# Kernel tuning notes

Hardware: AMD Instinct MI355X
Metric: run time of the kernel (lower is better)

The kernel has to match this reference:

```python
import jax, jax.numpy as jnp
import numpy as np

N = 100_000   # nodes
E = 1_600_000 # edges (avg degree 16)
D = 128       # numeric_dim
H = 128       # hidden_dim
C = 2         # num_classes
EPS = 1e-5    # BatchNorm eps


def setup_inputs() -> dict:
    key = jax.random.key(0)
    ks = jax.random.split(key, 24)

    def lin(k, i, o):  # torch Linear init-ish, stored as [in, out]
        return (jax.random.normal(k, (i, o), jnp.float32) / np.sqrt(i)).astype(jnp.float32)

    inp = {
        "x": jax.random.normal(ks[0], (N, D), jnp.float32),
        "edge_index": jax.random.randint(ks[1], (2, E), 0, N),
        "in_w": lin(ks[2], D, H),
        "in_b": jnp.zeros((H,), jnp.float32),
        "cls_w": lin(ks[3], H, C),
        "cls_b": jnp.zeros((C,), jnp.float32),
    }
    k = 4
    for blk in ("b1", "b2", "b3"):
        inp[f"{blk}_lw"] = lin(ks[k + 0], H, H)      # SAGEConv lin_l (aggregated neighbors), has bias
        inp[f"{blk}_lb"] = jnp.zeros((H,), jnp.float32)
        inp[f"{blk}_rw"] = lin(ks[k + 1], H, H)      # SAGEConv lin_r (root), bias=False in PyG
        inp[f"{blk}_g"] = jnp.ones((H,), jnp.float32)   # BN gamma
        inp[f"{blk}_bt"] = jnp.zeros((H,), jnp.float32)  # BN beta
        k += 2
    return inp


def _sage_block(x, src, dst, lw, lb, rw, g, bt):
    # SAGEConv with mean aggregation: messages flow src -> dst
    agg = jax.ops.segment_sum(x[src], dst, num_segments=N)            # [N, H]
    deg = jax.ops.segment_sum(jnp.ones((src.shape[0], 1), x.dtype), dst, num_segments=N)
    mean = agg / jnp.maximum(deg, 1.0)
    out = mean @ lw + lb + x @ rw                                     # lin_l(mean) + lin_r(x)
    # BatchNorm1d (training-mode batch stats over nodes), biased variance
    mu = out.mean(axis=0)
    var = out.var(axis=0)
    out = (out - mu) * jax.lax.rsqrt(var + EPS) * g + bt
    out = jax.nn.relu(out)
    # dropout in eval mode = identity; skip is Identity (H == H)
    return out + x


def reference(x, edge_index, in_w, in_b, cls_w, cls_b,
              b1_lw, b1_lb, b1_rw, b1_g, b1_bt,
              b2_lw, b2_lb, b2_rw, b2_g, b2_bt,
              b3_lw, b3_lb, b3_rw, b3_g, b3_bt):
    src, dst = edge_index[0], edge_index[1]
    h = jax.nn.relu(x @ in_w + in_b)
    h = _sage_block(h, src, dst, b1_lw, b1_lb, b1_rw, b1_g, b1_bt)
    h = _sage_block(h, src, dst, b2_lw, b2_lb, b2_rw, b2_g, b2_bt)
    h = _sage_block(h, src, dst, b3_lw, b3_lb, b3_rw, b3_g, b3_bt)
    return h @ cls_w + cls_b  # [N, C] logits
```

## Files before the change

### kernel.cpp

```cpp
#include <hip/hip_runtime.h>

#define NN 100000
#define NE 1600000
#define HD 128
#define EPSI 1e-5f

using u32 = unsigned int;
using u16 = unsigned short;

typedef short bf16x8 __attribute__((ext_vector_type(8)));
typedef float f32x4  __attribute__((ext_vector_type(4)));
typedef u32   u32x4  __attribute__((ext_vector_type(4)));

constexpr int SCAN_CHUNK  = 1024;
constexpr int SCAN_BLOCKS = (NN + SCAN_CHUNK - 1) / SCAN_CHUNK;
constexpr int NRANGE      = 128;
constexpr int RSZ2        = 784;
constexpr int BINCAP      = 16384;
constexpr int PART_CHUNK4 = 1024;
constexpr int PART_GRID   = (NE / 4 + PART_CHUNK4 - 1) / PART_CHUNK4;

__device__ inline float bflo(u32 u) { return __uint_as_float(u << 16); }
__device__ inline float bfhi(u32 u) { return __uint_as_float(u & 0xFFFF0000u); }
__device__ inline u16 f2bf(float f) {
    u32 u = __float_as_uint(f);
    u += 0x7FFFu + ((u >> 16) & 1u);
    return (u16)(u >> 16);
}
__device__ inline u32 pack2(float a, float b) {
    return (u32)f2bf(a) | ((u32)f2bf(b) << 16);
}


__global__ __launch_bounds__(256) void k_part(const int* __restrict__ src,
                                              const int* __restrict__ dst,
                                              int* __restrict__ binCur,
                                              u32* __restrict__ binbuf) {
    __shared__ int hist[NRANGE], base[NRANGE], curs[NRANGE];
    const int t  = threadIdx.x;
    const int c0 = blockIdx.x * PART_CHUNK4;
    if (t < NRANGE) { hist[t] = 0; curs[t] = 0; }
    __syncthreads();

    int4 ds[4], ss[4];
    bool ok[4];
#pragma unroll
    for (int i = 0; i < 4; ++i) {
        const int c = c0 + t + 256 * i;
        ok[i] = c < NE / 4;
        if (ok[i]) {
            ds[i] = reinterpret_cast<const int4*>(dst)[c];
            ss[i] = reinterpret_cast<const int4*>(src)[c];
        }
    }
#pragma unroll
    for (int i = 0; i < 4; ++i) {
        if (ok[i]) {
            atomicAdd(&hist[ds[i].x / RSZ2], 1);
            atomicAdd(&hist[ds[i].y / RSZ2], 1);
            atomicAdd(&hist[ds[i].z / RSZ2], 1);
            atomicAdd(&hist[ds[i].w / RSZ2], 1);
        }
    }
    __syncthreads();
    if (t < NRANGE && hist[t] > 0) base[t] = atomicAdd(&binCur[t], hist[t]);
    __syncthreads();

#pragma unroll
    for (int i = 0; i < 4; ++i) {
        if (ok[i]) {
            const int d[4] = {ds[i].x, ds[i].y, ds[i].z, ds[i].w};
            const int s[4] = {ss[i].x, ss[i].y, ss[i].z, ss[i].w};
#pragma unroll
            for (int j = 0; j < 4; ++j) {
                const int r  = d[j] / RSZ2;
                const int ld = d[j] - r * RSZ2;
                const int p  = base[r] + atomicAdd(&curs[r], 1);
                if (p < BINCAP)
                    binbuf[(size_t)r * BINCAP + p] = ((u32)s[j] << 10) | (u32)ld;
            }
        }
    }
}

__global__ __launch_bounds__(1024) void k_countL(const int* __restrict__ binCur,
                                                 const u32* __restrict__ binbuf,
                                                 int* __restrict__ cnt) {
    __shared__ int hist[RSZ2];
    const int b = blockIdx.x;
    const int t = threadIdx.x;
    for (int i = t; i < RSZ2; i += 1024) hist[i] = 0;
    __syncthreads();
    const int n = min(binCur[b], BINCAP);
    const u32* bin = binbuf + (size_t)b * BINCAP;
    for (int i = t; i < n; i += 1024)
        atomicAdd(&hist[bin[i] & 1023u], 1);
    __syncthreads();
    for (int i = t; i < RSZ2; i += 1024) {
        const int idx = b * RSZ2 + i;
        if (idx < NN) cnt[idx] = hist[i];
    }
}

__global__ void k_scan1(const int* __restrict__ cnt, int* __restrict__ rp,
                        int* __restrict__ tot) {
    __shared__ int lds[256];
    const int t    = threadIdx.x;
    const int base = blockIdx.x * SCAN_CHUNK + t * 4;
    int v[4];
#pragma unroll
    for (int i = 0; i < 4; ++i) v[i] = (base + i < NN) ? cnt[base + i] : 0;
    const int s = v[0] + v[1] + v[2] + v[3];
    lds[t] = s;
    __syncthreads();
    int val = s;
    for (int off = 1; off < 256; off <<= 1) {
        int other = (t >= off) ? lds[t - off] : 0;
        __syncthreads();
        val += other;
        lds[t] = val;
        __syncthreads();
    }
    int e = val - s;
#pragma unroll
    for (int i = 0; i < 4; ++i) {
        if (base + i < NN) rp[base + i] = e;
        e += v[i];
    }
    if (t == 255) tot[blockIdx.x] = val;
}

__global__ void k_scan2(int* __restrict__ tot, int* __restrict__ rp) {
    __shared__ int l[128];
    const int t = threadIdx.x;
    const int v = (t < SCAN_BLOCKS) ? tot[t] : 0;
    l[t] = v;
    __syncthreads();
    int val = v;
    for (int off = 1; off < 128; off <<= 1) {
        const int o = (t >= off) ? l[t - off] : 0;
        __syncthreads();
        val += o;
        l[t] = val;
        __syncthreads();
    }
    if (t < SCAN_BLOCKS) tot[t] = val - v;
    if (t == 127) rp[NN] = val;
}

__global__ void k_scan3(int* __restrict__ rp, const int* __restrict__ tot) {
    int idx = blockIdx.x * 256 + threadIdx.x;
    if (idx < NN) rp[idx] += tot[idx >> 10];
}

__global__ __launch_bounds__(1024) void k_fillL(const int* __restrict__ binCur,
                                                const u32* __restrict__ binbuf,
                                                const int* __restrict__ rp,
                                                int* __restrict__ col) {
    __shared__ int cur[RSZ2];
    const int b = blockIdx.x;
    const int t = threadIdx.x;
    for (int i = t; i < RSZ2; i += 1024) {
        const int idx = b * RSZ2 + i;
        cur[i] = (idx < NN) ? rp[idx] : 0;
    }
    __syncthreads();
    const int n = min(binCur[b], BINCAP);
    const u32* bin = binbuf + (size_t)b * BINCAP;
    for (int i = t; i < n; i += 1024) {
        const u32 e = bin[i];
        col[atomicAdd(&cur[e & 1023u], 1)] = (int)(e >> 10);
    }
}


struct WTArgs { const float* w[7]; u16* o[7]; };

__global__ void k_wt(WTArgs a) {
    const int m = blockIdx.y;
    const int n = blockIdx.x;
    const int k = threadIdx.x;
    a.o[m][n * HD + k] = f2bf(a.w[m][k * HD + n]);
}


__device__ inline void acc8(float* a, u32x4 v) {
    a[0] += bflo(v.x); a[1] += bfhi(v.x);
    a[2] += bflo(v.y); a[3] += bfhi(v.y);
    a[4] += bflo(v.z); a[5] += bfhi(v.z);
    a[6] += bflo(v.w); a[7] += bfhi(v.w);
}

__global__ __launch_bounds__(256) void k_agg(const u16* __restrict__ h,
                                             const int* __restrict__ rp,
                                             const int* __restrict__ col,
                                             u16* __restrict__ mean) {
    const int lane = threadIdx.x & 63;
    const int node = blockIdx.x * 4 + (threadIdx.x >> 6);
    const int grp  = lane >> 4;
    const int li   = lane & 15;
    const int r0 = rp[node], r1 = rp[node + 1];
    const size_t lof = (size_t)li * 8;
    float a[8];
#pragma unroll
    for (int i = 0; i < 8; ++i) a[i] = 0.f;
    int e = r0 + grp;
    for (; e + 12 < r1; e += 16) {
        const int s0 = col[e], s1 = col[e + 4], s2 = col[e + 8], s3 = col[e + 12];
        const u32x4 v0 = *reinterpret_cast<const u32x4*>(&h[(size_t)s0 * HD + lof]);
        const u32x4 v1 = *reinterpret_cast<const u32x4*>(&h[(size_t)s1 * HD + lof]);
        const u32x4 v2 = *reinterpret_cast<const u32x4*>(&h[(size_t)s2 * HD + lof]);
        const u32x4 v3 = *reinterpret_cast<const u32x4*>(&h[(size_t)s3 * HD + lof]);
        acc8(a, v0); acc8(a, v1); acc8(a, v2); acc8(a, v3);
    }
    for (; e < r1; e += 4) {
        const u32x4 v = *reinterpret_cast<const u32x4*>(&h[(size_t)col[e] * HD + lof]);
        acc8(a, v);
    }
#pragma unroll
    for (int i = 0; i < 8; ++i) {
        a[i] += __shfl_xor(a[i], 16);
        a[i] += __shfl_xor(a[i], 32);
    }
    if (lane < 16) {
        const float inv = 1.0f / fmaxf((float)(r1 - r0), 1.0f);
        u32x4 o;
        o.x = pack2(a[0] * inv, a[1] * inv);
        o.y = pack2(a[2] * inv, a[3] * inv);
        o.z = pack2(a[4] * inv, a[5] * inv);
        o.w = pack2(a[6] * inv, a[7] * inv);
        *reinterpret_cast<u32x4*>(&mean[(size_t)node * HD + lof]) = o;
    }
}


template <int A1F32, int RELU, int STATS>
__global__ __launch_bounds__(256) void k_mgemm(
    const void* __restrict__ A1p, const u16* __restrict__ W1T,
    const u16* __restrict__ A2, const u16* __restrict__ W2T,
    const float* __restrict__ bias, u16* __restrict__ out,
    float* __restrict__ stats)
{
    __shared__ u32x4 Wlds[2048];
    const int t    = threadIdx.x;
    const int wv   = t >> 6;
    const int lane = t & 63;
    const int lid  = lane & 15;
    const int kseg = lane >> 4;
    const int row0 = blockIdx.x * 128 + wv * 32;

    f32x4 acc[2][8];
#pragma unroll
    for (int rf = 0; rf < 2; ++rf)
#pragma unroll
        for (int c = 0; c < 8; ++c) acc[rf][c] = (f32x4){0.f, 0.f, 0.f, 0.f};

    int  ar[2];
    bool rok[2];
#pragma unroll
    for (int rf = 0; rf < 2; ++rf) {
        ar[rf]  = row0 + rf * 16 + lid;
        rok[rf] = ar[rf] < NN;
    }

#pragma unroll
    for (int i = 0; i < 8; ++i) {
        const int g   = t + 256 * i;
        const int row = g >> 4;
        const int ch  = g & 15;
        Wlds[row * 16 + (ch ^ (row & 7))] = reinterpret_cast<const u32x4*>(W1T)[g];
    }
    u32x4 wreg[8];
    if (A2 != nullptr) {
#pragma unroll
        for (int i = 0; i < 8; ++i)
            wreg[i] = reinterpret_cast<const u32x4*>(W2T)[t + 256 * i];
    }

    bf16x8 af1[2][4], af2[2][4];
    if (A1F32) {
        const float* A = (const float*)A1p;
#pragma unroll
        for (int rf = 0; rf < 2; ++rf)
#pragma unroll
            for (int kk = 0; kk < 4; ++kk) {
                const int kof = kk * 32 + kseg * 8;
                if (rok[rf]) {
                    const float4 f0 = *reinterpret_cast<const float4*>(&A[(size_t)ar[rf] * HD + kof]);
                    const float4 f1 = *reinterpret_cast<const float4*>(&A[(size_t)ar[rf] * HD + kof + 4]);
                    af1[rf][kk][0] = (short)f2bf(f0.x); af1[rf][kk][1] = (short)f2bf(f0.y);
                    af1[rf][kk][2] = (short)f2bf(f0.z); af1[rf][kk][3] = (short)f2bf(f0.w);
                    af1[rf][kk][4] = (short)f2bf(f1.x); af1[rf][kk][5] = (short)f2bf(f1.y);
                    af1[rf][kk][6] = (short)f2bf(f1.z); af1[rf][kk][7] = (short)f2bf(f1.w);
                } else {
                    af1[rf][kk] = (bf16x8)0;
                }
            }
    } else {
        const u16* A = (const u16*)A1p;
#pragma unroll
        for (int rf = 0; rf < 2; ++rf)
#pragma unroll
            for (int kk = 0; kk < 4; ++kk) {
                const int kof = kk * 32 + kseg * 8;
                af1[rf][kk] = rok[rf]
                    ? *reinterpret_cast<const bf16x8*>(&A[(size_t)ar[rf] * HD + kof])
                    : (bf16x8)0;
            }
    }
    if (A2 != nullptr) {
#pragma unroll
        for (int rf = 0; rf < 2; ++rf)
#pragma unroll
            for (int kk = 0; kk < 4; ++kk) {
                const int kof = kk * 32 + kseg * 8;
                af2[rf][kk] = rok[rf]
                    ? *reinterpret_cast<const bf16x8*>(&A2[(size_t)ar[rf] * HD + kof])
                    : (bf16x8)0;
            }
    }

    __syncthreads();
#pragma unroll
    for (int kk = 0; kk < 4; ++kk) {
#pragma unroll
        for (int c = 0; c < 8; ++c) {
            const int brow = c * 16 + lid;
            const bf16x8 bf = *reinterpret_cast<const bf16x8*>(
                &Wlds[brow * 16 + ((kk * 4 + kseg) ^ (lid & 7))]);
#pragma unroll
            for (int rf = 0; rf < 2; ++rf)
                acc[rf][c] = __builtin_amdgcn_mfma_f32_16x16x32_bf16(af1[rf][kk], bf, acc[rf][c], 0, 0, 0);
        }
    }

    if (A2 != nullptr) {
        __syncthreads();
#pragma unroll
        for (int i = 0; i < 8; ++i) {
            const int g   = t + 256 * i;
            const int row = g >> 4;
            const int ch  = g & 15;
            Wlds[row * 16 + (ch ^ (row & 7))] = wreg[i];
        }
        __syncthreads();
#pragma unroll
        for (int kk = 0; kk < 4; ++kk) {
#pragma unroll
            for (int c = 0; c < 8; ++c) {
                const int brow = c * 16 + lid;
                const bf16x8 bf = *reinterpret_cast<const bf16x8*>(
                    &Wlds[brow * 16 + ((kk * 4 + kseg) ^ (lid & 7))]);
#pragma unroll
                for (int rf = 0; rf < 2; ++rf)
                    acc[rf][c] = __builtin_amdgcn_mfma_f32_16x16x32_bf16(af2[rf][kk], bf, acc[rf][c], 0, 0, 0);
            }
        }
    }

    float bv[8];
#pragma unroll
    for (int c = 0; c < 8; ++c) bv[c] = bias[c * 16 + lid];

    float sv[8], qv[8];
#pragma unroll
    for (int c = 0; c < 8; ++c) { sv[c] = 0.f; qv[c] = 0.f; }

#pragma unroll
    for (int rf = 0; rf < 2; ++rf) {
#pragma unroll
        for (int c = 0; c < 8; ++c) {
            const int colc = c * 16 + lid;
#pragma unroll
            for (int j = 0; j < 4; ++j) {
                const int rrow = row0 + rf * 16 + kseg * 4 + j;
                if (rrow < NN) {
                    float o = acc[rf][c][j] + bv[c];
                    if (RELU) o = fmaxf(o, 0.f);
                    out[(size_t)rrow * HD + colc] = f2bf(o);
                    sv[c] += o;
                    qv[c] += o * o;
                }
            }
        }
    }

    if constexpr (STATS) {
        __shared__ float ls[4][HD], lq[4][HD];
#pragma unroll
        for (int c = 0; c < 8; ++c) {
            sv[c] += __shfl_xor(sv[c], 16);
            sv[c] += __shfl_xor(sv[c], 32);
            qv[c] += __shfl_xor(qv[c], 16);
            qv[c] += __shfl_xor(qv[c], 32);
        }
        if (lane < 16) {
#pragma unroll
            for (int c = 0; c < 8; ++c) {
                ls[wv][c * 16 + lid] = sv[c];
                lq[wv][c * 16 + lid] = qv[c];
            }
        }
        __syncthreads();
        if (t < HD) {
            const float s = (ls[0][t] + ls[1][t]) + (ls[2][t] + ls[3][t]);
            atomicAdd(&stats[t], s);
        } else {
            const int j = t - HD;
            const float q = (lq[0][j] + lq[1][j]) + (lq[2][j] + lq[3][j]);
            atomicAdd(&stats[HD + j], q);
        }
    }
}


template <int CLS>
__global__ __launch_bounds__(256) void k_apply(
    const u16* __restrict__ outb, const float* __restrict__ stats,
    const float* __restrict__ g, const float* __restrict__ bt,
    u16* __restrict__ hb, const float* __restrict__ cw,
    const float* __restrict__ cb, float* __restrict__ logits)
{
    const int t = threadIdx.x;
    const size_t idx4 = (size_t)blockIdx.x * 256 + t;
    const int j = (int)(idx4 & 31) * 4;
    const float4 svv = *reinterpret_cast<const float4*>(&stats[j]);
    const float4 qvv = *reinterpret_cast<const float4*>(&stats[HD + j]);
    const float4 gv  = *reinterpret_cast<const float4*>(&g[j]);
    const float4 bv  = *reinterpret_cast<const float4*>(&bt[j]);
    const float invn = 1.0f / (float)NN;
    float sc[4], sh[4];
    {
        const float sa[4] = {svv.x, svv.y, svv.z, svv.w};
        const float qa[4] = {qvv.x, qvv.y, qvv.z, qvv.w};
        const float ga[4] = {gv.x, gv.y, gv.z, gv.w};
        const float ba[4] = {bv.x, bv.y, bv.z, bv.w};
#pragma unroll
        for (int i = 0; i < 4; ++i) {
            const float mean = sa[i] * invn;
            const float var  = qa[i] * invn - mean * mean;
            sc[i] = ga[i] * rsqrtf(var + EPSI);
            sh[i] = ba[i] - mean * sc[i];
        }
    }
    const uint2 o  = reinterpret_cast<const uint2*>(outb)[idx4];
    const uint2 hv = reinterpret_cast<const uint2*>(hb)[idx4];
    const float r0 = fmaxf(bflo(o.x) * sc[0] + sh[0], 0.f) + bflo(hv.x);
    const float r1 = fmaxf(bfhi(o.x) * sc[1] + sh[1], 0.f) + bfhi(hv.x);
    const float r2 = fmaxf(bflo(o.y) * sc[2] + sh[2], 0.f) + bflo(hv.y);
    const float r3 = fmaxf(bfhi(o.y) * sc[3] + sh[3], 0.f) + bfhi(hv.y);
    reinterpret_cast<uint2*>(hb)[idx4] = make_uint2(pack2(r0, r1), pack2(r2, r3));

    if constexpr (CLS) {
        const float4 w01 = *reinterpret_cast<const float4*>(&cw[j * 2]);
        const float4 w23 = *reinterpret_cast<const float4*>(&cw[j * 2 + 4]);
        float p0 = r0 * w01.x + r1 * w01.z + r2 * w23.x + r3 * w23.z;
        float p1 = r0 * w01.y + r1 * w01.w + r2 * w23.y + r3 * w23.w;
#pragma unroll
        for (int off = 1; off <= 16; off <<= 1) {
            p0 += __shfl_xor(p0, off);
            p1 += __shfl_xor(p1, off);
        }
        if ((t & 31) == 0) {
            const size_t row = idx4 >> 5;
            logits[row * 2 + 0] = p0 + cb[0];
            logits[row * 2 + 1] = p1 + cb[1];
        }
    }
}


extern "C" void kernel_launch(void* const* d_in, const int* in_sizes, int n_in,
                              void* d_out, int out_size, void* d_ws, size_t ws_size,
                              hipStream_t stream) {
    const float* x     = (const float*)d_in[0];
    const int*   ei    = (const int*)d_in[1];
    const float* in_w  = (const float*)d_in[2];
    const float* in_b  = (const float*)d_in[3];
    const float* cls_w = (const float*)d_in[4];
    const float* cls_b = (const float*)d_in[5];
    const float* blk_w[3][5];
    for (int bidx = 0; bidx < 3; ++bidx)
        for (int k = 0; k < 5; ++k)
            blk_w[bidx][k] = (const float*)d_in[6 + bidx * 5 + k];

    const int* src = ei;
    const int* dst = ei + NE;

    size_t off = 0;
    auto alloc = [&](size_t bytes) {
        void* p = (char*)d_ws + off;
        off += (bytes + 255) & ~(size_t)255;
        return p;
    };
    u16*   h      = (u16*)alloc((size_t)NN * HD * 2);
    u16*   tmp    = (u16*)alloc((size_t)NN * HD * 2);
    int*   rp     = (int*)alloc((size_t)(NN + 1) * 4);
    int*   cnt    = (int*)alloc((size_t)NN * 4);
    int*   col    = (int*)alloc((size_t)NE * 4);
    int*   stot   = (int*)alloc((size_t)SCAN_BLOCKS * 4);
    u16*   wtb    = (u16*)alloc((size_t)7 * HD * HD * 2);
    const size_t off_z = off;
    float* stats  = (float*)alloc((size_t)3 * 256 * 4);
    int*   binCur = (int*)alloc((size_t)NRANGE * 4);
    const size_t zspan = off - off_z;
    u32*   binbuf = (u32*)tmp;
    (void)ws_size; (void)n_in; (void)in_sizes; (void)out_size;

    (void)hipMemsetAsync(stats, 0, zspan, stream);

    WTArgs wa;
    wa.w[0] = in_w;
    for (int bidx = 0; bidx < 3; ++bidx) {
        wa.w[1 + bidx * 2] = blk_w[bidx][0];
        wa.w[2 + bidx * 2] = blk_w[bidx][2];
    }
    for (int m = 0; m < 7; ++m) wa.o[m] = wtb + (size_t)m * HD * HD;
    k_wt<<<dim3(HD, 7), HD, 0, stream>>>(wa);

    k_part<<<PART_GRID, 256, 0, stream>>>(src, dst, binCur, binbuf);
    k_countL<<<NRANGE, 1024, 0, stream>>>(binCur, binbuf, cnt);
    k_scan1<<<SCAN_BLOCKS, 256, 0, stream>>>(cnt, rp, stot);
    k_scan2<<<1, 128, 0, stream>>>(stot, rp);
    k_scan3<<<(NN + 255) / 256, 256, 0, stream>>>(rp, stot);
    k_fillL<<<NRANGE, 1024, 0, stream>>>(binCur, binbuf, rp, col);

    const int gemm_grid  = (NN + 127) / 128;
    const int apply_grid = NN * 32 / 256;

    k_mgemm<1, 1, 0><<<gemm_grid, 256, 0, stream>>>(x, wtb, nullptr, nullptr, in_b, h, nullptr);

    for (int bidx = 0; bidx < 3; ++bidx) {
        const u16* lwT = wtb + (size_t)(1 + bidx * 2) * HD * HD;
        const u16* rwT = wtb + (size_t)(2 + bidx * 2) * HD * HD;
        const float* lb = blk_w[bidx][1];
        const float* g  = blk_w[bidx][3];
        const float* bt = blk_w[bidx][4];
        float* st = stats + bidx * 256;
        k_agg<<<NN / 4, 256, 0, stream>>>(h, rp, col, tmp);
        k_mgemm<0, 0, 1><<<gemm_grid, 256, 0, stream>>>(tmp, lwT, h, rwT, lb, tmp, st);
        if (bidx < 2)
            k_apply<0><<<apply_grid, 256, 0, stream>>>(tmp, st, g, bt, h,
                                                       nullptr, nullptr, nullptr);
        else
            k_apply<1><<<apply_grid, 256, 0, stream>>>(tmp, st, g, bt, h,
                                                       cls_w, cls_b, (float*)d_out);
    }
}
```

Measured before the change: 397.3 us.

## Fuse neighbor mean aggregation into SAGE GEMM kernel via LDS staging

Replaces the separate aggregation kernel and the dual GEMM with one kernel. Each block gathers and averages neighbor rows for its 128 nodes into LDS, then runs both MFMA GEMMs. This removes the write and re-read of the bf16 mean tensor and one launch per block. In exchange, the gather now runs on only about 782 blocks with each wave handling 32 nodes in sequence, so fewer loads are in flight. LDS use also rises to about 68KB per block, which can cut occupancy during the latency-bound gather phase.

After: 659.5 us. 1.66x slower.

```diff
diff --git a/kernel.cpp b/kernel.cpp
--- a/kernel.cpp
+++ b/kernel.cpp
@@ -191,55 +191,10 @@
     a[6] += bflo(v.w); a[7] += bfhi(v.w);
 }
 
-__global__ __launch_bounds__(256) void k_agg(const u16* __restrict__ h,
-                                             const int* __restrict__ rp,
-                                             const int* __restrict__ col,
-                                             u16* __restrict__ mean) {
-    const int lane = threadIdx.x & 63;
-    const int node = blockIdx.x * 4 + (threadIdx.x >> 6);
-    const int grp  = lane >> 4;
-    const int li   = lane & 15;
-    const int r0 = rp[node], r1 = rp[node + 1];
-    const size_t lof = (size_t)li * 8;
-    float a[8];
-#pragma unroll
-    for (int i = 0; i < 8; ++i) a[i] = 0.f;
-    int e = r0 + grp;
-    for (; e + 12 < r1; e += 16) {
-        const int s0 = col[e], s1 = col[e + 4], s2 = col[e + 8], s3 = col[e + 12];
-        const u32x4 v0 = *reinterpret_cast<const u32x4*>(&h[(size_t)s0 * HD + lof]);
-        const u32x4 v1 = *reinterpret_cast<const u32x4*>(&h[(size_t)s1 * HD + lof]);
-        const u32x4 v2 = *reinterpret_cast<const u32x4*>(&h[(size_t)s2 * HD + lof]);
-        const u32x4 v3 = *reinterpret_cast<const u32x4*>(&h[(size_t)s3 * HD + lof]);
-        acc8(a, v0); acc8(a, v1); acc8(a, v2); acc8(a, v3);
-    }
-    for (; e < r1; e += 4) {
-        const u32x4 v = *reinterpret_cast<const u32x4*>(&h[(size_t)col[e] * HD + lof]);
-        acc8(a, v);
-    }
-#pragma unroll
-    for (int i = 0; i < 8; ++i) {
-        a[i] += __shfl_xor(a[i], 16);
-        a[i] += __shfl_xor(a[i], 32);
-    }
-    if (lane < 16) {
-        const float inv = 1.0f / fmaxf((float)(r1 - r0), 1.0f);
-        u32x4 o;
-        o.x = pack2(a[0] * inv, a[1] * inv);
-        o.y = pack2(a[2] * inv, a[3] * inv);
-        o.z = pack2(a[4] * inv, a[5] * inv);
-        o.w = pack2(a[6] * inv, a[7] * inv);
-        *reinterpret_cast<u32x4*>(&mean[(size_t)node * HD + lof]) = o;
-    }
-}
-
-
-template <int A1F32, int RELU, int STATS>
-__global__ __launch_bounds__(256) void k_mgemm(
-    const void* __restrict__ A1p, const u16* __restrict__ W1T,
-    const u16* __restrict__ A2, const u16* __restrict__ W2T,
-    const float* __restrict__ bias, u16* __restrict__ out,
-    float* __restrict__ stats)
+
+__global__ __launch_bounds__(256) void k_mgemm_in(
+    const float* __restrict__ A, const u16* __restrict__ W1T,
+    const float* __restrict__ bias, u16* __restrict__ out)
 {
     __shared__ u32x4 Wlds[2048];
     const int t    = threadIdx.x;
@@ -270,55 +225,24 @@
         const int ch  = g & 15;
         Wlds[row * 16 + (ch ^ (row & 7))] = reinterpret_cast<const u32x4*>(W1T)[g];
     }
-    u32x4 wreg[8];
-    if (A2 != nullptr) {
-#pragma unroll
-        for (int i = 0; i < 8; ++i)
-            wreg[i] = reinterpret_cast<const u32x4*>(W2T)[t + 256 * i];
-    }
-
-    bf16x8 af1[2][4], af2[2][4];
-    if (A1F32) {
-        const float* A = (const float*)A1p;
-#pragma unroll
-        for (int rf = 0; rf < 2; ++rf)
-#pragma unroll
-            for (int kk = 0; kk < 4; ++kk) {
-                const int kof = kk * 32 + kseg * 8;
-                if (rok[rf]) {
-                    const float4 f0 = *reinterpret_cast<const float4*>(&A[(size_t)ar[rf] * HD + kof]);
-                    const float4 f1 = *reinterpret_cast<const float4*>(&A[(size_t)ar[rf] * HD + kof + 4]);
-                    af1[rf][kk][0] = (short)f2bf(f0.x); af1[rf][kk][1] = (short)f2bf(f0.y);
-                    af1[rf][kk][2] = (short)f2bf(f0.z); af1[rf][kk][3] = (short)f2bf(f0.w);
-                    af1[rf][kk][4] = (short)f2bf(f1.x); af1[rf][kk][5] = (short)f2bf(f1.y);
-                    af1[rf][kk][6] = (short)f2bf(f1.z); af1[rf][kk][7] = (short)f2bf(f1.w);
-                } else {
-                    af1[rf][kk] = (bf16x8)0;
-                }
-            }
-    } else {
-        const u16* A = (const u16*)A1p;
-#pragma unroll
-        for (int rf = 0; rf < 2; ++rf)
-#pragma unroll
-            for (int kk = 0; kk < 4; ++kk) {
-                const int kof = kk * 32 + kseg * 8;
-                af1[rf][kk] = rok[rf]
-                    ? *reinterpret_cast<const bf16x8*>(&A[(size_t)ar[rf] * HD + kof])
-                    : (bf16x8)0;
-            }
-    }
-    if (A2 != nullptr) {
-#pragma unroll
-        for (int rf = 0; rf < 2; ++rf)
-#pragma unroll
-            for (int kk = 0; kk < 4; ++kk) {
-                const int kof = kk * 32 + kseg * 8;
-                af2[rf][kk] = rok[rf]
-                    ? *reinterpret_cast<const bf16x8*>(&A2[(size_t)ar[rf] * HD + kof])
-                    : (bf16x8)0;
-            }
-    }
+
+    bf16x8 af[2][4];
+#pragma unroll
+    for (int rf = 0; rf < 2; ++rf)
+#pragma unroll
+        for (int kk = 0; kk < 4; ++kk) {
+            const int kof = kk * 32 + kseg * 8;
+            if (rok[rf]) {
+                const float4 f0 = *reinterpret_cast<const float4*>(&A[(size_t)ar[rf] * HD + kof]);
+                const float4 f1 = *reinterpret_cast<const float4*>(&A[(size_t)ar[rf] * HD + kof + 4]);
+                af[rf][kk][0] = (short)f2bf(f0.x); af[rf][kk][1] = (short)f2bf(f0.y);
+                af[rf][kk][2] = (short)f2bf(f0.z); af[rf][kk][3] = (short)f2bf(f0.w);
+                af[rf][kk][4] = (short)f2bf(f1.x); af[rf][kk][5] = (short)f2bf(f1.y);
+                af[rf][kk][6] = (short)f2bf(f1.z); af[rf][kk][7] = (short)f2bf(f1.w);
+            } else {
+                af[rf][kk] = (bf16x8)0;
+            }
+        }
 
     __syncthreads();
 #pragma unroll
@@ -330,31 +254,167 @@
                 &Wlds[brow * 16 + ((kk * 4 + kseg) ^ (lid & 7))]);
 #pragma unroll
             for (int rf = 0; rf < 2; ++rf)
+                acc[rf][c] = __builtin_amdgcn_mfma_f32_16x16x32_bf16(af[rf][kk], bf, acc[rf][c], 0, 0, 0);
+        }
+    }
+
+#pragma unroll
+    for (int rf = 0; rf < 2; ++rf) {
+#pragma unroll
+        for (int c = 0; c < 8; ++c) {
+            const int colc = c * 16 + lid;
+            const float bv = bias[colc];
+#pragma unroll
+            for (int j = 0; j < 4; ++j) {
+                const int rrow = row0 + rf * 16 + kseg * 4 + j;
+                if (rrow < NN)
+                    out[(size_t)rrow * HD + colc] = f2bf(fmaxf(acc[rf][c][j] + bv, 0.f));
+            }
+        }
+    }
+}
+
+
+__global__ __launch_bounds__(256) void k_msage(
+    const u16* __restrict__ h, const int* __restrict__ rp,
+    const int* __restrict__ col,
+    const u16* __restrict__ W1T, const u16* __restrict__ W2T,
+    const float* __restrict__ bias, u16* __restrict__ out,
+    float* __restrict__ stats)
+{
+    __shared__ u32x4 Wlds[2048];
+    __shared__ u32x4 Mlds[2048];
+    __shared__ float ls[4][HD], lq[4][HD];
+    const int t    = threadIdx.x;
+    const int wv   = t >> 6;
+    const int lane = t & 63;
+    const int lid  = lane & 15;
+    const int kseg = lane >> 4;
+    const int row0 = blockIdx.x * 128 + wv * 32;
+
+    u32x4 w1reg[8], w2reg[8];
+#pragma unroll
+    for (int i = 0; i < 8; ++i) w1reg[i] = reinterpret_cast<const u32x4*>(W1T)[t + 256 * i];
+#pragma unroll
+    for (int i = 0; i < 8; ++i) w2reg[i] = reinterpret_cast<const u32x4*>(W2T)[t + 256 * i];
+
+    const size_t lof = (size_t)lid * 8;
+    for (int i = 0; i < 32; ++i) {
+        const int node = row0 + i;
+        const int lrow = wv * 32 + i;
+        if (node < NN) {
+            const int r0 = rp[node], r1 = rp[node + 1];
+            float a[8];
+#pragma unroll
+            for (int k = 0; k < 8; ++k) a[k] = 0.f;
+            int e = r0 + kseg;
+            for (; e + 12 < r1; e += 16) {
+                const int s0 = col[e], s1 = col[e + 4], s2 = col[e + 8], s3 = col[e + 12];
+                const u32x4 v0 = *reinterpret_cast<const u32x4*>(&h[(size_t)s0 * HD + lof]);
+                const u32x4 v1 = *reinterpret_cast<const u32x4*>(&h[(size_t)s1 * HD + lof]);
+                const u32x4 v2 = *reinterpret_cast<const u32x4*>(&h[(size_t)s2 * HD + lof]);
+                const u32x4 v3 = *reinterpret_cast<const u32x4*>(&h[(size_t)s3 * HD + lof]);
+                acc8(a, v0); acc8(a, v1); acc8(a, v2); acc8(a, v3);
+            }
+            for (; e < r1; e += 4) {
+                const u32x4 v = *reinterpret_cast<const u32x4*>(&h[(size_t)col[e] * HD + lof]);
+                acc8(a, v);
+            }
+#pragma unroll
+            for (int k = 0; k < 8; ++k) {
+                a[k] += __shfl_xor(a[k], 16);
+                a[k] += __shfl_xor(a[k], 32);
+            }
+            if (lane < 16) {
+                const float inv = 1.0f / fmaxf((float)(r1 - r0), 1.0f);
+                u32x4 o;
+                o.x = pack2(a[0] * inv, a[1] * inv);
+                o.y = pack2(a[2] * inv, a[3] * inv);
+                o.z = pack2(a[4] * inv, a[5] * inv);
+                o.w = pack2(a[6] * inv, a[7] * inv);
+                Mlds[lrow * 16 + (lane ^ (lrow & 7))] = o;
+            }
+        } else if (lane < 16) {
+            Mlds[lrow * 16 + (lane ^ (lrow & 7))] = (u32x4){0u, 0u, 0u, 0u};
+        }
+    }
+
+#pragma unroll
+    for (int i = 0; i < 8; ++i) {
+        const int g   = t + 256 * i;
+        const int row = g >> 4;
+        const int ch  = g & 15;
+        Wlds[row * 16 + (ch ^ (row & 7))] = w1reg[i];
+    }
+
+    int  ar[2];
+    bool rok[2];
+#pragma unroll
+    for (int rf = 0; rf < 2; ++rf) {
+        ar[rf]  = row0 + rf * 16 + lid;
+        rok[rf] = ar[rf] < NN;
+    }
+
+    bf16x8 af2[2][4];
+#pragma unroll
+    for (int rf = 0; rf < 2; ++rf)
+#pragma unroll
+        for (int kk = 0; kk < 4; ++kk) {
+            const int kof = kk * 32 + kseg * 8;
+            af2[rf][kk] = rok[rf]
+                ? *reinterpret_cast<const bf16x8*>(&h[(size_t)ar[rf] * HD + kof])
+                : (bf16x8)0;
+        }
+
+    bf16x8 af1[2][4];
+#pragma unroll
+    for (int rf = 0; rf < 2; ++rf)
+#pragma unroll
+        for (int kk = 0; kk < 4; ++kk) {
+            const int lrow = wv * 32 + rf * 16 + lid;
+            af1[rf][kk] = *reinterpret_cast<const bf16x8*>(
+                &Mlds[lrow * 16 + ((kk * 4 + kseg) ^ (lid & 7))]);
+        }
+
+    f32x4 acc[2][8];
+#pragma unroll
+    for (int rf = 0; rf < 2; ++rf)
+#pragma unroll
+        for (int c = 0; c < 8; ++c) acc[rf][c] = (f32x4){0.f, 0.f, 0.f, 0.f};
+
+    __syncthreads();
+#pragma unroll
+    for (int kk = 0; kk < 4; ++kk) {
+#pragma unroll
+        for (int c = 0; c < 8; ++c) {
+            const int brow = c * 16 + lid;
+            const bf16x8 bf = *reinterpret_cast<const bf16x8*>(
+                &Wlds[brow * 16 + ((kk * 4 + kseg) ^ (lid & 7))]);
+#pragma unroll
+            for (int rf = 0; rf < 2; ++rf)
                 acc[rf][c] = __builtin_amdgcn_mfma_f32_16x16x32_bf16(af1[rf][kk], bf, acc[rf][c], 0, 0, 0);
         }
     }
 
-    if (A2 != nullptr) {
-        __syncthreads();
-#pragma unroll
-        for (int i = 0; i < 8; ++i) {
-            const int g   = t + 256 * i;
-            const int row = g >> 4;
-            const int ch  = g & 15;
-            Wlds[row * 16 + (ch ^ (row & 7))] = wreg[i];
-        }
-        __syncthreads();
-#pragma unroll
-        for (int kk = 0; kk < 4; ++kk) {
-#pragma unroll
-            for (int c = 0; c < 8; ++c) {
-                const int brow = c * 16 + lid;
-                const bf16x8 bf = *reinterpret_cast<const bf16x8*>(
-                    &Wlds[brow * 16 + ((kk * 4 + kseg) ^ (lid & 7))]);
-#pragma unroll
-                for (int rf = 0; rf < 2; ++rf)
-                    acc[rf][c] = __builtin_amdgcn_mfma_f32_16x16x32_bf16(af2[rf][kk], bf, acc[rf][c], 0, 0, 0);
-            }
+    __syncthreads();
+#pragma unroll
+    for (int i = 0; i < 8; ++i) {
+        const int g   = t + 256 * i;
+        const int row = g >> 4;
+        const int ch  = g & 15;
+        Wlds[row * 16 + (ch ^ (row & 7))] = w2reg[i];
+    }
+    __syncthreads();
+#pragma unroll
+    for (int kk = 0; kk < 4; ++kk) {
+#pragma unroll
+        for (int c = 0; c < 8; ++c) {
+            const int brow = c * 16 + lid;
+            const bf16x8 bf = *reinterpret_cast<const bf16x8*>(
+                &Wlds[brow * 16 + ((kk * 4 + kseg) ^ (lid & 7))]);
+#pragma unroll
+            for (int rf = 0; rf < 2; ++rf)
+                acc[rf][c] = __builtin_amdgcn_mfma_f32_16x16x32_bf16(af2[rf][kk], bf, acc[rf][c], 0, 0, 0);
         }
     }
 
@@ -375,8 +435,7 @@
             for (int j = 0; j < 4; ++j) {
                 const int rrow = row0 + rf * 16 + kseg * 4 + j;
                 if (rrow < NN) {
-                    float o = acc[rf][c][j] + bv[c];
-                    if (RELU) o = fmaxf(o, 0.f);
+                    const float o = acc[rf][c][j] + bv[c];
                     out[(size_t)rrow * HD + colc] = f2bf(o);
                     sv[c] += o;
                     qv[c] += o * o;
@@ -385,31 +444,28 @@
         }
     }
 
-    if constexpr (STATS) {
-        __shared__ float ls[4][HD], lq[4][HD];
+#pragma unroll
+    for (int c = 0; c < 8; ++c) {
+        sv[c] += __shfl_xor(sv[c], 16);
+        sv[c] += __shfl_xor(sv[c], 32);
+        qv[c] += __shfl_xor(qv[c], 16);
+        qv[c] += __shfl_xor(qv[c], 32);
+    }
+    if (lane < 16) {
 #pragma unroll
         for (int c = 0; c < 8; ++c) {
-            sv[c] += __shfl_xor(sv[c], 16);
-            sv[c] += __shfl_xor(sv[c], 32);
-            qv[c] += __shfl_xor(qv[c], 16);
-            qv[c] += __shfl_xor(qv[c], 32);
-        }
-        if (lane < 16) {
-#pragma unroll
-            for (int c = 0; c < 8; ++c) {
-                ls[wv][c * 16 + lid] = sv[c];
-                lq[wv][c * 16 + lid] = qv[c];
-            }
-        }
-        __syncthreads();
-        if (t < HD) {
-            const float s = (ls[0][t] + ls[1][t]) + (ls[2][t] + ls[3][t]);
-            atomicAdd(&stats[t], s);
-        } else {
-            const int j = t - HD;
-            const float q = (lq[0][j] + lq[1][j]) + (lq[2][j] + lq[3][j]);
-            atomicAdd(&stats[HD + j], q);
-        }
+            ls[wv][c * 16 + lid] = sv[c];
+            lq[wv][c * 16 + lid] = qv[c];
+        }
+    }
+    __syncthreads();
+    if (t < HD) {
+        const float s = (ls[0][t] + ls[1][t]) + (ls[2][t] + ls[3][t]);
+        atomicAdd(&stats[t], s);
+    } else {
+        const int j = t - HD;
+        const float q = (lq[0][j] + lq[1][j]) + (lq[2][j] + lq[3][j]);
+        atomicAdd(&stats[HD + j], q);
     }
 }
 
@@ -528,7 +584,7 @@
     const int gemm_grid  = (NN + 127) / 128;
     const int apply_grid = NN * 32 / 256;
 
-    k_mgemm<1, 1, 0><<<gemm_grid, 256, 0, stream>>>(x, wtb, nullptr, nullptr, in_b, h, nullptr);
+    k_mgemm_in<<<gemm_grid, 256, 0, stream>>>(x, wtb, in_b, h);
 
     for (int bidx = 0; bidx < 3; ++bidx) {
         const u16* lwT = wtb + (size_t)(1 + bidx * 2) * HD * HD;
@@ -537,8 +593,7 @@
         const float* g  = blk_w[bidx][3];
         const float* bt = blk_w[bidx][4];
         float* st = stats + bidx * 256;
-        k_agg<<<NN / 4, 256, 0, stream>>>(h, rp, col, tmp);
-        k_mgemm<0, 0, 1><<<gemm_grid, 256, 0, stream>>>(tmp, lwT, h, rwT, lb, tmp, st);
+        k_msage<<<gemm_grid, 256, 0, stream>>>(h, rp, col, lwT, rwT, lb, tmp, st);
         if (bidx < 2)
             k_apply<0><<<apply_grid, 256, 0, stream>>>(tmp, st, g, bt, h,
                                                        nullptr, nullptr, nullptr);
```

## Fuse CSR count, scan and fill into one binned kernel

Applied to the files above, without the earlier changes.

Replaces the five-kernel CSR build (per-bin histogram, three-stage global scan, fill) with a single kernel. Each block first scans the per-bin edge totals to find its global base, then builds a local histogram and scans it in LDS to produce row pointers before scattering column indices. This removes four launches and the global count/scan round trips. The mean aggregation output is also written with nontemporal stores. In exchange, every block redundantly scans the bin totals, and the local scan uses a 1024-step barrier-heavy Hillis-Steele pass.

New measurement: 392.3 us. Within noise of the previous version (-1.3%).

```diff
diff --git a/kernel.cpp b/kernel.cpp
--- a/kernel.cpp
+++ b/kernel.cpp
@@ -12,8 +12,6 @@
 typedef float f32x4  __attribute__((ext_vector_type(4)));
 typedef u32   u32x4  __attribute__((ext_vector_type(4)));
 
-constexpr int SCAN_CHUNK  = 1024;
-constexpr int SCAN_BLOCKS = (NN + SCAN_CHUNK - 1) / SCAN_CHUNK;
 constexpr int NRANGE      = 128;
 constexpr int RSZ2        = 784;
 constexpr int BINCAP      = 16384;
@@ -83,93 +81,55 @@
     }
 }
 
-__global__ __launch_bounds__(1024) void k_countL(const int* __restrict__ binCur,
+__global__ __launch_bounds__(1024) void k_fillL2(const int* __restrict__ binCur,
                                                  const u32* __restrict__ binbuf,
-                                                 int* __restrict__ cnt) {
-    __shared__ int hist[RSZ2];
+                                                 int* __restrict__ rp,
+                                                 int* __restrict__ col) {
+    __shared__ int hist[1024];
+    __shared__ int sbuf[1024];
+    __shared__ int bscan[NRANGE];
     const int b = blockIdx.x;
     const int t = threadIdx.x;
-    for (int i = t; i < RSZ2; i += 1024) hist[i] = 0;
-    __syncthreads();
+
+    hist[t] = 0;
+    if (t < NRANGE) bscan[t] = min(binCur[t], BINCAP);
+    __syncthreads();
+
+    int bval = (t < NRANGE) ? bscan[t] : 0;
+    for (int off = 1; off < NRANGE; off <<= 1) {
+        const int o = (t >= off && t < NRANGE) ? bscan[t - off] : 0;
+        __syncthreads();
+        bval += o;
+        if (t < NRANGE) bscan[t] = bval;
+        __syncthreads();
+    }
+    const int binbase = (b == 0) ? 0 : bscan[b - 1];
+
     const int n = min(binCur[b], BINCAP);
     const u32* bin = binbuf + (size_t)b * BINCAP;
     for (int i = t; i < n; i += 1024)
         atomicAdd(&hist[bin[i] & 1023u], 1);
     __syncthreads();
-    for (int i = t; i < RSZ2; i += 1024) {
-        const int idx = b * RSZ2 + i;
-        if (idx < NN) cnt[idx] = hist[i];
-    }
-}
-
-__global__ void k_scan1(const int* __restrict__ cnt, int* __restrict__ rp,
-                        int* __restrict__ tot) {
-    __shared__ int lds[256];
-    const int t    = threadIdx.x;
-    const int base = blockIdx.x * SCAN_CHUNK + t * 4;
-    int v[4];
-#pragma unroll
-    for (int i = 0; i < 4; ++i) v[i] = (base + i < NN) ? cnt[base + i] : 0;
-    const int s = v[0] + v[1] + v[2] + v[3];
-    lds[t] = s;
-    __syncthreads();
-    int val = s;
-    for (int off = 1; off < 256; off <<= 1) {
-        int other = (t >= off) ? lds[t - off] : 0;
-        __syncthreads();
-        val += other;
-        lds[t] = val;
-        __syncthreads();
-    }
-    int e = val - s;
-#pragma unroll
-    for (int i = 0; i < 4; ++i) {
-        if (base + i < NN) rp[base + i] = e;
-        e += v[i];
-    }
-    if (t == 255) tot[blockIdx.x] = val;
-}
-
-__global__ void k_scan2(int* __restrict__ tot, int* __restrict__ rp) {
-    __shared__ int l[128];
-    const int t = threadIdx.x;
-    const int v = (t < SCAN_BLOCKS) ? tot[t] : 0;
-    l[t] = v;
-    __syncthreads();
-    int val = v;
-    for (int off = 1; off < 128; off <<= 1) {
-        const int o = (t >= off) ? l[t - off] : 0;
-        __syncthreads();
-        val += o;
-        l[t] = val;
-        __syncthreads();
-    }
-    if (t < SCAN_BLOCKS) tot[t] = val - v;
-    if (t == 127) rp[NN] = val;
-}
-
-__global__ void k_scan3(int* __restrict__ rp, const int* __restrict__ tot) {
-    int idx = blockIdx.x * 256 + threadIdx.x;
-    if (idx < NN) rp[idx] += tot[idx >> 10];
-}
-
-__global__ __launch_bounds__(1024) void k_fillL(const int* __restrict__ binCur,
-                                                const u32* __restrict__ binbuf,
-                                                const int* __restrict__ rp,
-                                                int* __restrict__ col) {
-    __shared__ int cur[RSZ2];
-    const int b = blockIdx.x;
-    const int t = threadIdx.x;
-    for (int i = t; i < RSZ2; i += 1024) {
-        const int idx = b * RSZ2 + i;
-        cur[i] = (idx < NN) ? rp[idx] : 0;
-    }
-    __syncthreads();
-    const int n = min(binCur[b], BINCAP);
-    const u32* bin = binbuf + (size_t)b * BINCAP;
+
+    int v = hist[t];
+    for (int off = 1; off < 1024; off <<= 1) {
+        sbuf[t] = v;
+        __syncthreads();
+        if (t >= off) v += sbuf[t - off];
+        __syncthreads();
+    }
+    const int excl = v - hist[t];
+    const int rpv  = binbase + excl;
+    const int idx  = b * RSZ2 + t;
+    if (t < RSZ2 && idx < NN) rp[idx] = rpv;
+    if (b == NRANGE - 1 && t == 0) rp[NN] = bscan[NRANGE - 1];
+    __syncthreads();
+    hist[t] = rpv;
+    __syncthreads();
+
     for (int i = t; i < n; i += 1024) {
         const u32 e = bin[i];
-        col[atomicAdd(&cur[e & 1023u], 1)] = (int)(e >> 10);
+        col[atomicAdd(&hist[e & 1023u], 1)] = (int)(e >> 10);
     }
 }
 
@@ -229,7 +189,7 @@
         o.y = pack2(a[2] * inv, a[3] * inv);
         o.z = pack2(a[4] * inv, a[5] * inv);
         o.w = pack2(a[6] * inv, a[7] * inv);
-        *reinterpret_cast<u32x4*>(&mean[(size_t)node * HD + lof]) = o;
+        __builtin_nontemporal_store(o, reinterpret_cast<u32x4*>(&mean[(size_t)node * HD + lof]));
     }
 }
 
@@ -496,9 +456,7 @@
     u16*   h      = (u16*)alloc((size_t)NN * HD * 2);
     u16*   tmp    = (u16*)alloc((size_t)NN * HD * 2);
     int*   rp     = (int*)alloc((size_t)(NN + 1) * 4);
-    int*   cnt    = (int*)alloc((size_t)NN * 4);
     int*   col    = (int*)alloc((size_t)NE * 4);
-    int*   stot   = (int*)alloc((size_t)SCAN_BLOCKS * 4);
     u16*   wtb    = (u16*)alloc((size_t)7 * HD * HD * 2);
     const size_t off_z = off;
     float* stats  = (float*)alloc((size_t)3 * 256 * 4);
@@ -519,11 +477,7 @@
     k_wt<<<dim3(HD, 7), HD, 0, stream>>>(wa);
 
     k_part<<<PART_GRID, 256, 0, stream>>>(src, dst, binCur, binbuf);
-    k_countL<<<NRANGE, 1024, 0, stream>>>(binCur, binbuf, cnt);
-    k_scan1<<<SCAN_BLOCKS, 256, 0, stream>>>(cnt, rp, stot);
-    k_scan2<<<1, 128, 0, stream>>>(stot, rp);
-    k_scan3<<<(NN + 255) / 256, 256, 0, stream>>>(rp, stot);
-    k_fillL<<<NRANGE, 1024, 0, stream>>>(binCur, binbuf, rp, col);
+    k_fillL2<<<NRANGE, 1024, 0, stream>>>(binCur, binbuf, rp, col);
 
     const int gemm_grid  = (NN + 127) / 128;
     const int apply_grid = NN * 32 / 256;
```
